# Kernel optimization log

Hardware: AMD Instinct MI355X
Metric: run time of the kernel (lower is better)

The kernel has to match this reference:

```python
import jax, jax.numpy as jnp
import numpy as np

IMG = 40  # imgSize hard-coded in FFTNet


def _fft_layer(z, w):
    # z: complex64 [B, inC, H, W]; w: float32 [inC, outC, H, W, 2]
    # torch.fft(..., 2, normalized=True) == 2D FFT with 'ortho' norm over last two dims
    F = jnp.fft.fft2(z, norm='ortho')
    wc = jax.lax.complex(w[..., 0], w[..., 1])
    # dft_conv: per-frequency complex multiply then sum over input channels
    # (Karatsuba trick in the original == plain complex multiply)
    mixed = jnp.einsum('bihw,iohw->bohw', F, wc)
    return jnp.fft.ifft2(mixed, norm='ortho')


def _crelu(z):
    # F.relu applied to the stacked [..., 2] real/imag tensor => relu each part
    return jax.lax.complex(jax.nn.relu(z.real), jax.nn.relu(z.imag))


def _fftnet(x, ws):
    # x: [B, 1, H, W] real; stacked with zeros -> complex input
    z = x.astype(jnp.complex64)
    for w in ws[:-1]:
        z = _crelu(_fft_layer(z, w))
    z = _fft_layer(z, ws[-1])
    return z.real  # x[..., 0]


def setup_inputs() -> dict:
    key = jax.random.key(0)
    ks = jax.random.split(key, 7)
    B = 256
    x = jax.random.normal(ks[0], (B, 1, IMG, IMG), dtype=jnp.float32)

    def make_w(k, i, o):
        # xavier_normal_ on torch shape (1, i, o, H, W, 2):
        # fan_in = i * (o*H*W*2), fan_out = 1 * (o*H*W*2)
        recept = o * IMG * IMG * 2
        std = float(np.sqrt(2.0 / (i * recept + recept)))
        return jax.random.normal(k, (i, o, IMG, IMG, 2), dtype=jnp.float32) * std

    chans = [(1, 40), (40, 40), (40, 40), (40, 40), (40, 40), (40, 1)]
    inp = {'x': x}
    for n, (k, (i, o)) in enumerate(zip(ks[1:], chans), start=1):
        inp[f'w{n}'] = make_w(k, i, o)
    return inp


def reference(x, w1, w2, w3, w4, w5, w6):
    return _fftnet(x, (w1, w2, w3, w4, w5, w6))
```

## Files before the change

kernel.cpp:

```cpp
#include <hip/hip_runtime.h>
#include <math.h>

#define NPIX 1600
#define NIMG 40
#define SW   40
#define PSZ  (48 * SW)

#define RST 322
#define OST 482

typedef __bf16 bf16x8 __attribute__((ext_vector_type(8)));
typedef float  f32x4  __attribute__((ext_vector_type(4)));
#define MFMA __builtin_amdgcn_mfma_f32_16x16x32_bf16

__device__ __forceinline__ unsigned short bits16(__bf16 x) {
    return __builtin_bit_cast(unsigned short, x);
}

__device__ __forceinline__ void cfma(float2& acc, float ax, float ay, float bx, float by) {
    acc.x = fmaf(ax, bx, fmaf(-ay, by, acc.x));
    acc.y = fmaf(ax, by, fmaf( ay, bx, acc.y));
}

__global__ void init_dtab(unsigned short* __restrict__ Dtab) {
    int idx = blockIdx.x * 256 + threadIdx.x;
    if (idx >= 2304) return;
    int rec = idx >> 6, lane = idx & 63;
    int p = rec % 6, t = (rec / 6) % 3, kc = rec / 18;
    unsigned short out[8];
    for (int j = 0; j < 8; ++j) {
        int k = kc * 32 + (lane >> 4) * 8 + j;
        int n = t * 16 + (lane & 15);
        float val = 0.0f;
        if (k < 40 && n < 40) {
            float ang = 6.28318530717958647692f * (float)((k * n) % 40) / 40.0f;
            float dr, di, s, c;
            sincosf(ang, &s, &c);
            dr = c; di = s;
            float base = (p < 2) ? dr : (p < 4) ? di : -di;
            __bf16 hi = (__bf16)base;
            if ((p & 1) == 0) val = (float)hi;
            else              val = (float)(__bf16)(base - (float)hi);
        }
        out[j] = __builtin_bit_cast(unsigned short, (__bf16)val);
    }
    unsigned short* dst = Dtab + (size_t)rec * 512 + lane * 8;
    for (int j = 0; j < 8; ++j) dst[j] = out[j];
}

template<bool REAL_IN, bool RELU, bool REAL_OUT>
__global__ __launch_bounds__(256) void fft2_kernel(const void* __restrict__ inv,
                                                   void* __restrict__ outv,
                                                   int dir)
{
    const int img = blockIdx.x;
    const int tid = threadIdx.x;
    __shared__ float2 A[NPIX];
    __shared__ float2 T[NPIX];
    __shared__ float2 D[NPIX];
    __shared__ float2 tw[NIMG];

    if (tid < NIMG) {
        float ang = (float)dir * 6.28318530717958647692f * (float)tid / 40.0f;
        float s, c;
        sincosf(ang, &s, &c);
        tw[tid] = make_float2(c, s);
    }
    if (REAL_IN) {
        const float* in = (const float*)inv + (size_t)img * NPIX;
        for (int idx = tid; idx < NPIX; idx += 256)
            A[idx] = make_float2(in[idx], 0.0f);
    } else {
        const float2* in = (const float2*)inv + (size_t)img * NPIX;
        for (int idx = tid; idx < NPIX; idx += 256)
            A[idx] = in[idx];
    }
    __syncthreads();
    for (int idx = tid; idx < NPIX; idx += 256) {
        int a = idx / NIMG, b = idx - a * NIMG;
        D[idx] = tw[(a * b) % NIMG];
    }
    __syncthreads();

    for (int idx = tid; idx < NPIX; idx += 256) {
        int h = idx / NIMG, v = idx - h * NIMG;
        float2 s = make_float2(0.0f, 0.0f);
        const float2* Arow = &A[h * NIMG];
        #pragma unroll
        for (int w = 0; w < NIMG; ++w) {
            float2 a = Arow[w];
            float2 d = D[w * NIMG + v];
            s.x += a.x * d.x - a.y * d.y;
            s.y += a.x * d.y + a.y * d.x;
        }
        T[idx] = s;
    }
    __syncthreads();

    for (int idx = tid; idx < NPIX; idx += 256) {
        int u = idx / NIMG, v = idx - u * NIMG;
        float2 s = make_float2(0.0f, 0.0f);
        const float2* Du = &D[u * NIMG];
        #pragma unroll
        for (int h = 0; h < NIMG; ++h) {
            float2 t = T[h * NIMG + v];
            float2 d = Du[h];
            s.x += t.x * d.x - t.y * d.y;
            s.y += t.x * d.y + t.y * d.x;
        }
        s.x *= 0.025f;
        s.y *= 0.025f;
        if (RELU) { s.x = fmaxf(s.x, 0.0f); s.y = fmaxf(s.y, 0.0f); }
        if (REAL_OUT) {
            ((float*)outv)[(size_t)img * NPIX + idx] = s.x;
        } else {
            ((float2*)outv)[(size_t)img * NPIX + idx] = s;
        }
    }
}

__device__ __forceinline__ void mac_row(f32x4& aR, f32x4& aI,
    bf16x8 xrh, bf16x8 xrl, bf16x8 xih, bf16x8 xil,
    bf16x8 drh, bf16x8 drl, bf16x8 dih, bf16x8 dil, bf16x8 dnh, bf16x8 dnl)
{
    aR = MFMA(xrh, drh, aR, 0, 0, 0);
    aR = MFMA(xrl, drh, aR, 0, 0, 0);
    aR = MFMA(xrh, drl, aR, 0, 0, 0);
    aR = MFMA(xih, dnh, aR, 0, 0, 0);
    aR = MFMA(xil, dnh, aR, 0, 0, 0);
    aR = MFMA(xih, dnl, aR, 0, 0, 0);
    aI = MFMA(xrh, dih, aI, 0, 0, 0);
    aI = MFMA(xrl, dih, aI, 0, 0, 0);
    aI = MFMA(xrh, dil, aI, 0, 0, 0);
    aI = MFMA(xih, drh, aI, 0, 0, 0);
    aI = MFMA(xil, drh, aI, 0, 0, 0);
    aI = MFMA(xih, drl, aI, 0, 0, 0);
}

__device__ __forceinline__ void mac_col(f32x4& aR, f32x4& aI,
    bf16x8 drh, bf16x8 drl, bf16x8 dih, bf16x8 dil, bf16x8 dnh, bf16x8 dnl,
    bf16x8 trh, bf16x8 trl, bf16x8 tih, bf16x8 til)
{
    aR = MFMA(drh, trh, aR, 0, 0, 0);
    aR = MFMA(drl, trh, aR, 0, 0, 0);
    aR = MFMA(drh, trl, aR, 0, 0, 0);
    aR = MFMA(dnh, tih, aR, 0, 0, 0);
    aR = MFMA(dnl, tih, aR, 0, 0, 0);
    aR = MFMA(dnh, til, aR, 0, 0, 0);
    aI = MFMA(drh, tih, aI, 0, 0, 0);
    aI = MFMA(drl, tih, aI, 0, 0, 0);
    aI = MFMA(drh, til, aI, 0, 0, 0);
    aI = MFMA(dih, trh, aI, 0, 0, 0);
    aI = MFMA(dil, trh, aI, 0, 0, 0);
    aI = MFMA(dih, trl, aI, 0, 0, 0);
}

__device__ __forceinline__ void mac_mix(f32x4& aR, f32x4& aI,
    bf16x8 frh, bf16x8 frl, bf16x8 fih, bf16x8 fil, bf16x8 fnih, bf16x8 fnil,
    bf16x8 wrh, bf16x8 wrl, bf16x8 wih, bf16x8 wil)
{
    aR = MFMA(frh,  wrh, aR, 0, 0, 0);
    aR = MFMA(frl,  wrh, aR, 0, 0, 0);
    aR = MFMA(frh,  wrl, aR, 0, 0, 0);
    aR = MFMA(fnih, wih, aR, 0, 0, 0);
    aR = MFMA(fnil, wih, aR, 0, 0, 0);
    aR = MFMA(fnih, wil, aR, 0, 0, 0);
    aI = MFMA(frh,  wih, aI, 0, 0, 0);
    aI = MFMA(frl,  wih, aI, 0, 0, 0);
    aI = MFMA(frh,  wil, aI, 0, 0, 0);
    aI = MFMA(fih,  wrh, aI, 0, 0, 0);
    aI = MFMA(fil,  wrh, aI, 0, 0, 0);
    aI = MFMA(fih,  wrl, aI, 0, 0, 0);
}

__global__ __launch_bounds__(512, 2) void mix_mfma_kernel(const float2* __restrict__ F,
                                                          const float2* __restrict__ W,
                                                          float2* __restrict__ M)
{
    __shared__ alignas(16) char smem[102912];
    float2* raw  = (float2*)smem;
    float2* outt = (float2*)(smem + 41216);
    float2* lw   = (float2*)smem;

    const int tid  = threadIdx.x;
    const int w    = tid >> 6;
    const int lane = tid & 63;
    const int q    = lane >> 4;
    const int m    = lane & 15;
    const int fw   = blockIdx.x >> 3;
    const int bg   = blockIdx.x & 7;
    const int f0   = fw * 8;
    const int fsub = w;

    f32x4 pf[5];
    #pragma unroll
    for (int k = 0; k < 5; ++k) {
        int c = tid + (k << 9);
        int r = c >> 2, sub = c & 3;
        int b = r / 40, i = r - b * 40;
        const f32x4* g = (const f32x4*)(F + ((size_t)((bg * 32 + b) * 40 + i) * NPIX + f0));
        pf[k] = __builtin_nontemporal_load(g + sub);
    }

    #pragma unroll
    for (int k = 0; k < 13; ++k) {
        int c = tid + (k << 9);
        if (c < 6400) {
            int r = c >> 2, sub = c & 3;
            const f32x4* g = (const f32x4*)(W + ((size_t)r * NPIX + f0));
            *(f32x4*)&lw[r * 8 + sub * 2] = g[sub];
        }
    }
    __syncthreads();

    bf16x8 wt[2][3][4];
    #pragma unroll
    for (int kc = 0; kc < 2; ++kc) {
        #pragma unroll
        for (int nt = 0; nt < 3; ++nt) {
            bf16x8 wrh = (bf16x8){}, wrl = (bf16x8){};
            bf16x8 wih = (bf16x8){}, wil = (bf16x8){};
            const int o = nt * 16 + m;
            const bool have = ((kc == 0) || (q == 0)) && (o < 40);
            if (have) {
                #pragma unroll
                for (int j = 0; j < 8; ++j) {
                    int i = kc * 32 + q * 8 + j;
                    float2 v = lw[(i * 40 + o) * 8 + fsub];
                    __bf16 h1 = (__bf16)v.x;
                    wrh[j] = h1; wrl[j] = (__bf16)(v.x - (float)h1);
                    __bf16 h2 = (__bf16)v.y;
                    wih[j] = h2; wil[j] = (__bf16)(v.y - (float)h2);
                }
            }
            wt[kc][nt][0] = wrh; wt[kc][nt][1] = wrl;
            wt[kc][nt][2] = wih; wt[kc][nt][3] = wil;
        }
    }
    __syncthreads();

    #pragma unroll
    for (int bt = 0; bt < 2; ++bt) {
        const int btile = bg * 2 + bt;

        #pragma unroll
        for (int k = 0; k < 5; ++k) {
            int c = tid + (k << 9);
            int r = c >> 2, sub = c & 3;
            int b = r / 40, i = r - b * 40;
            *(f32x4*)&raw[b * RST + i * 8 + sub * 2] = pf[k];
        }
        __syncthreads();

        if (bt == 0) {
            #pragma unroll
            for (int k = 0; k < 5; ++k) {
                int c = tid + (k << 9);
                int r = c >> 2, sub = c & 3;
                int b = r / 40, i = r - b * 40;
                const f32x4* g = (const f32x4*)(F + ((size_t)(((bg * 2 + 1) * 16 + b) * 40 + i) * NPIX + f0));
                pf[k] = __builtin_nontemporal_load(g + sub);
            }
        }

        f32x4 accR[3], accI[3];
        #pragma unroll
        for (int nt = 0; nt < 3; ++nt) {
            accR[nt] = (f32x4){0.f, 0.f, 0.f, 0.f};
            accI[nt] = (f32x4){0.f, 0.f, 0.f, 0.f};
        }

        #pragma unroll
        for (int kc = 0; kc < 2; ++kc) {
            const bool have = (kc == 0) || (q == 0);
            float re[8], im[8];
            #pragma unroll
            for (int j = 0; j < 8; ++j) {
                int i = kc * 32 + q * 8 + j;
                if (have) {
                    float2 v = raw[m * RST + i * 8 + fsub];
                    re[j] = v.x; im[j] = v.y;
                } else { re[j] = 0.f; im[j] = 0.f; }
            }
            bf16x8 frh, frl, fih, fil, fnih, fnil;
            #pragma unroll
            for (int j = 0; j < 8; ++j) {
                __bf16 h1 = (__bf16)re[j];
                frh[j] = h1;
                float lo = re[j] - (float)h1;
                frl[j] = (__bf16)lo;
                __bf16 h2 = (__bf16)im[j];
                fih[j] = h2;
                float lo2 = im[j] - (float)h2;
                fil[j] = (__bf16)lo2;
                fnih[j] = (__bf16)(-(float)h2);
                fnil[j] = (__bf16)(-lo2);
            }
            #pragma unroll
            for (int nt = 0; nt < 3; ++nt)
                mac_mix(accR[nt], accI[nt], frh, frl, fih, fil, fnih, fnil,
                        wt[kc][nt][0], wt[kc][nt][1], wt[kc][nt][2], wt[kc][nt][3]);
        }

        #pragma unroll
        for (int nt = 0; nt < 3; ++nt)
            #pragma unroll
            for (int g2 = 0; g2 < 4; ++g2)
                outt[(q * 4 + g2) * OST + (nt * 16 + m) * 10 + fsub] =
                    make_float2(accR[nt][g2], accI[nt][g2]);
        __syncthreads();

        #pragma unroll
        for (int k = 0; k < 5; ++k) {
            int c = tid + (k << 9);
            int r = c >> 2, sub = c & 3;
            int b = r / 40, o = r - b * 40;
            f32x4 v = *(const f32x4*)&outt[b * OST + o * 10 + sub * 2];
            f32x4* g = (f32x4*)(M + ((size_t)((btile * 16 + b) * 40 + o) * NPIX + f0));
            __builtin_nontemporal_store(v, g + sub);
        }
    }
}

__global__ __launch_bounds__(576, 5) void fused_mfma_kernel(const float2* __restrict__ in,
                                                            float2* __restrict__ outg,
                                                            const unsigned short* __restrict__ Dtab)
{
    __shared__ unsigned short Pl[4 * PSZ];
    __shared__ unsigned short Dlds[36 * 512];

    const int tid  = threadIdx.x;
    const int wv   = tid >> 6;
    const int lane = tid & 63;
    const int q    = lane >> 4;
    const int m    = lane & 15;
    const int mt   = wv / 3;
    const int nt   = wv - mt * 3;

    #pragma unroll
    for (int c = 0; c < 4; ++c) {
        int idx = c * 576 + tid;
        int rec = idx >> 6, l2 = idx & 63;
        *(f32x4*)&Dlds[rec * 512 + l2 * 8] =
            *(const f32x4*)(Dtab + (size_t)rec * 512 + l2 * 8);
    }

    #pragma unroll 1
    for (int ii = 0; ii < 5; ++ii) {
        const size_t img  = (size_t)blockIdx.x + (size_t)ii * 2048;
        const size_t base = img * NPIX;

        {
            const float4* src = (const float4*)(in + base);
            #pragma unroll
            for (int c = 0; c < 2; ++c) {
                int p = c * 576 + tid;
                if (p < 800) {
                    float4 v = src[p];
                    int h = p / 20, w2 = (p - h * 20) * 2;
                    int o = h * SW + w2;
                    __bf16 rh0 = (__bf16)v.x, ih0 = (__bf16)v.y;
                    __bf16 rh1 = (__bf16)v.z, ih1 = (__bf16)v.w;
                    ushort2 s0, s1, s2, s3;
                    s0.x = bits16(rh0); s0.y = bits16(rh1);
                    s1.x = bits16((__bf16)(v.x - (float)rh0));
                    s1.y = bits16((__bf16)(v.z - (float)rh1));
                    s2.x = bits16(ih0); s2.y = bits16(ih1);
                    s3.x = bits16((__bf16)(v.y - (float)ih0));
                    s3.y = bits16((__bf16)(v.w - (float)ih1));
                    *(ushort2*)&Pl[0 * PSZ + o] = s0;
                    *(ushort2*)&Pl[1 * PSZ + o] = s1;
                    *(ushort2*)&Pl[2 * PSZ + o] = s2;
                    *(ushort2*)&Pl[3 * PSZ + o] = s3;
                }
            }
            if (tid < 320) {
                int pl = tid / 80, rem = tid - pl * 80;
                int r = 40 + rem / 10, c4 = (rem - (rem / 10) * 10) * 4;
                *(ushort4*)&Pl[pl * PSZ + r * SW + c4] = make_ushort4(0, 0, 0, 0);
            }
        }
        __syncthreads();

        #pragma unroll
        for (int rep = 0; rep < 2; ++rep) {
            const int IP = rep ? 4 : 2;
            const int IN = rep ? 2 : 4;

            f32x4 aR = (f32x4){0.f, 0.f, 0.f, 0.f};
            f32x4 aI = (f32x4){0.f, 0.f, 0.f, 0.f};

            #pragma unroll
            for (int kc = 0; kc < 2; ++kc) {
                const bool have = (kc == 0) || (q == 0);
                bf16x8 xrh, xrl, xih, xil;
                if (have) {
                    int o = (mt * 16 + m) * SW + kc * 32 + q * 8;
                    xrh = *(const bf16x8*)&Pl[0 * PSZ + o];
                    xrl = *(const bf16x8*)&Pl[1 * PSZ + o];
                    xih = *(const bf16x8*)&Pl[2 * PSZ + o];
                    xil = *(const bf16x8*)&Pl[3 * PSZ + o];
                } else {
                    xrh = (bf16x8){}; xrl = (bf16x8){};
                    xih = (bf16x8){}; xil = (bf16x8){};
                }
                const int rb = (kc * 3 + nt) * 6;
                bf16x8 drh = *(const bf16x8*)&Dlds[(rb + 0) * 512 + lane * 8];
                bf16x8 drl = *(const bf16x8*)&Dlds[(rb + 1) * 512 + lane * 8];
                bf16x8 dih = *(const bf16x8*)&Dlds[(rb + IP) * 512 + lane * 8];
                bf16x8 dil = *(const bf16x8*)&Dlds[(rb + IP + 1) * 512 + lane * 8];
                bf16x8 dnh = *(const bf16x8*)&Dlds[(rb + IN) * 512 + lane * 8];
                bf16x8 dnl = *(const bf16x8*)&Dlds[(rb + IN + 1) * 512 + lane * 8];
                __builtin_amdgcn_s_setprio(1);
                mac_row(aR, aI, xrh, xrl, xih, xil,
                        drh, drl, dih, dil, dnh, dnl);
                __builtin_amdgcn_s_setprio(0);
            }
            __syncthreads();

            {
                int hb = mt * 16 + q * 4;
                if (hb < 40) {
                    int v = nt * 16 + m;
                    ushort4 srh, srl, sih, sil;
                    unsigned short* prh = (unsigned short*)&srh;
                    unsigned short* prl = (unsigned short*)&srl;
                    unsigned short* pih = (unsigned short*)&sih;
                    unsigned short* pil = (unsigned short*)&sil;
                    #pragma unroll
                    for (int g = 0; g < 4; ++g) {
                        __bf16 h1 = (__bf16)aR[g];
                        prh[g] = bits16(h1);
                        prl[g] = bits16((__bf16)(aR[g] - (float)h1));
                        __bf16 h2 = (__bf16)aI[g];
                        pih[g] = bits16(h2);
                        pil[g] = bits16((__bf16)(aI[g] - (float)h2));
                    }
                    int o = v * SW + hb;
                    *(ushort4*)&Pl[0 * PSZ + o] = srh;
                    *(ushort4*)&Pl[1 * PSZ + o] = srl;
                    *(ushort4*)&Pl[2 * PSZ + o] = sih;
                    *(ushort4*)&Pl[3 * PSZ + o] = sil;
                }
            }
            __syncthreads();

            aR = (f32x4){0.f, 0.f, 0.f, 0.f};
            aI = (f32x4){0.f, 0.f, 0.f, 0.f};

            #pragma unroll
            for (int kc = 0; kc < 2; ++kc) {
                const bool have = (kc == 0) || (q == 0);
                bf16x8 trh, trl, tih, til;
                if (have) {
                    int o = (nt * 16 + m) * SW + kc * 32 + q * 8;
                    trh = *(const bf16x8*)&Pl[0 * PSZ + o];
                    trl = *(const bf16x8*)&Pl[1 * PSZ + o];
                    tih = *(const bf16x8*)&Pl[2 * PSZ + o];
                    til = *(const bf16x8*)&Pl[3 * PSZ + o];
                } else {
                    trh = (bf16x8){}; trl = (bf16x8){};
                    tih = (bf16x8){}; til = (bf16x8){};
                }
                const int rb = (kc * 3 + mt) * 6;
                bf16x8 drh = *(const bf16x8*)&Dlds[(rb + 0) * 512 + lane * 8];
                bf16x8 drl = *(const bf16x8*)&Dlds[(rb + 1) * 512 + lane * 8];
                bf16x8 dih = *(const bf16x8*)&Dlds[(rb + IP) * 512 + lane * 8];
                bf16x8 dil = *(const bf16x8*)&Dlds[(rb + IP + 1) * 512 + lane * 8];
                bf16x8 dnh = *(const bf16x8*)&Dlds[(rb + IN) * 512 + lane * 8];
                bf16x8 dnl = *(const bf16x8*)&Dlds[(rb + IN + 1) * 512 + lane * 8];
                __builtin_amdgcn_s_setprio(1);
                mac_col(aR, aI, drh, drl, dih, dil, dnh, dnl,
                        trh, trl, tih, til);
                __builtin_amdgcn_s_setprio(0);
            }

            if (rep == 0) {
                __syncthreads();
                int v = nt * 16 + m;
                int u0 = mt * 16 + q * 4;
                if (v < 40 && u0 < 40) {
                    ushort4 srh, srl, sih, sil;
                    unsigned short* prh = (unsigned short*)&srh;
                    unsigned short* prl = (unsigned short*)&srl;
                    unsigned short* pih = (unsigned short*)&sih;
                    unsigned short* pil = (unsigned short*)&sil;
                    #pragma unroll
                    for (int g = 0; g < 4; ++g) {
                        float xr = fmaxf(aR[g] * 0.025f, 0.f);
                        float xi = fmaxf(aI[g] * 0.025f, 0.f);
                        __bf16 h1 = (__bf16)xr;
                        prh[g] = bits16(h1);
                        prl[g] = bits16((__bf16)(xr - (float)h1));
                        __bf16 h2 = (__bf16)xi;
                        pih[g] = bits16(h2);
                        pil[g] = bits16((__bf16)(xi - (float)h2));
                    }
                    int o = v * SW + u0;
                    *(ushort4*)&Pl[0 * PSZ + o] = srh;
                    *(ushort4*)&Pl[1 * PSZ + o] = srl;
                    *(ushort4*)&Pl[2 * PSZ + o] = sih;
                    *(ushort4*)&Pl[3 * PSZ + o] = sil;
                }
                __syncthreads();
            } else {
                float2* dst = outg + base;
                int v = nt * 16 + m;
                int u0 = mt * 16 + q * 4;
                if (v < 40 && u0 < 40) {
                    float4 s0, s1;
                    s0.x = aR[0] * 0.025f; s0.y = aI[0] * 0.025f;
                    s0.z = aR[1] * 0.025f; s0.w = aI[1] * 0.025f;
                    s1.x = aR[2] * 0.025f; s1.y = aI[2] * 0.025f;
                    s1.z = aR[3] * 0.025f; s1.w = aI[3] * 0.025f;
                    *(float4*)&dst[v * NIMG + u0]     = s0;
                    *(float4*)&dst[v * NIMG + u0 + 2] = s1;
                }
            }
        }
        __syncthreads();
    }
}

template<int INC, int OUTC, int BT, int OT>
__global__ __launch_bounds__(256) void mix_kernel(const float2* __restrict__ F,
                                                  const float2* __restrict__ W,
                                                  float2* __restrict__ M)
{
    const int tid = threadIdx.x;
    const int lane = tid & 63;
    const int wv = tid >> 6;
    const int f = (blockIdx.x % 25) * 64 + lane;
    const int bg = (blockIdx.x / 25) * 4 + wv;
    const int b0 = bg * BT;

    #pragma unroll
    for (int o0 = 0; o0 < OUTC; o0 += OT) {
        float2 acc[BT][OT];
        #pragma unroll
        for (int t = 0; t < BT; ++t)
            #pragma unroll
            for (int o = 0; o < OT; ++o)
                acc[t][o] = make_float2(0.0f, 0.0f);

        for (int i = 0; i < INC; ++i) {
            float2 fv[BT];
            #pragma unroll
            for (int t = 0; t < BT; ++t)
                fv[t] = F[((size_t)(b0 + t) * INC + i) * NPIX + f];
            float2 wr[OT];
            #pragma unroll
            for (int o = 0; o < OT; ++o)
                wr[o] = W[((size_t)i * OUTC + (o0 + o)) * NPIX + f];
            #pragma unroll
            for (int t = 0; t < BT; ++t)
                #pragma unroll
                for (int o = 0; o < OT; ++o)
                    cfma(acc[t][o], fv[t].x, fv[t].y, wr[o].x, wr[o].y);
        }
        #pragma unroll
        for (int t = 0; t < BT; ++t)
            #pragma unroll
            for (int o = 0; o < OT; ++o)
                M[((size_t)(b0 + t) * OUTC + (o0 + o)) * NPIX + f] = acc[t][o];
    }
}

extern "C" void kernel_launch(void* const* d_in, const int* in_sizes, int n_in,
                              void* d_out, int out_size, void* d_ws, size_t ws_size,
                              hipStream_t stream)
{
    const float* x = (const float*)d_in[0];
    const float2* w[6];
    for (int i = 0; i < 6; ++i) w[i] = (const float2*)d_in[1 + i];
    float* out = (float*)d_out;

    const size_t bufBytes = (size_t)256 * 40 * NPIX * sizeof(float2);
    float2* A = (float2*)d_ws;
    float2* B = (float2*)((char*)d_ws + bufBytes);
    unsigned short* Dtab = (unsigned short*)((char*)d_ws + 2 * bufBytes);

    const int FUSEGRID = 2048;
    const int MIXBLK = 25 * (256 / 4) / 4;

    init_dtab<<<9, 256, 0, stream>>>(Dtab);

    fft2_kernel<true, false, false><<<256, 256, 0, stream>>>(x, A, -1);

    mix_kernel<1, 40, 4, 10><<<MIXBLK, 256, 0, stream>>>(A, w[0], B);
    fused_mfma_kernel<<<FUSEGRID, 576, 0, stream>>>(B, A, Dtab);

    for (int l = 1; l <= 4; ++l) {
        mix_mfma_kernel<<<1600, 512, 0, stream>>>(A, w[l], B);
        fused_mfma_kernel<<<FUSEGRID, 576, 0, stream>>>(B, A, Dtab);
    }

    mix_kernel<40, 1, 4, 1><<<MIXBLK, 256, 0, stream>>>(A, w[5], B);
    fft2_kernel<false, false, true><<<256, 256, 0, stream>>>(B, out, +1);
}
```

Before: 1.415 ms.

## Keep DFT twiddle fragments in registers and split complex MACs into four real accumulators

The fused FFT kernel no longer stages the DFT twiddle table in shared memory. Each wave loads its eight bf16 twiddle fragments (hi/lo of real and imaginary parts) into registers once. The forward and inverse transforms now reuse those fragments through four separate real-product accumulators, and signs are combined at store time, so the negated-imaginary table and the per-iteration LDS loads are no longer needed. The wave-to-tile mapping is changed so the same twiddle fragment serves both row and column passes. This lowers LDS traffic and footprint at the cost of more VGPRs, and the launch bound drops from 5 to 4 blocks per CU.

Measured after the change: 1.384 ms. -2.2%, faster.

```diff
diff --git a/kernel.cpp b/kernel.cpp
--- a/kernel.cpp
+++ b/kernel.cpp
@@ -20,6 +20,14 @@
 __device__ __forceinline__ void cfma(float2& acc, float ax, float ay, float bx, float by) {
     acc.x = fmaf(ax, bx, fmaf(-ay, by, acc.x));
     acc.y = fmaf(ax, by, fmaf( ay, bx, acc.y));
+}
+
+__device__ __forceinline__ void mac3(f32x4& acc, bf16x8 ah, bf16x8 al,
+                                     bf16x8 bh, bf16x8 bl)
+{
+    acc = MFMA(ah, bh, acc, 0, 0, 0);
+    acc = MFMA(al, bh, acc, 0, 0, 0);
+    acc = MFMA(ah, bl, acc, 0, 0, 0);
 }
 
 __global__ void init_dtab(unsigned short* __restrict__ Dtab) {
@@ -119,42 +127,6 @@
     }
 }
 
-__device__ __forceinline__ void mac_row(f32x4& aR, f32x4& aI,
-    bf16x8 xrh, bf16x8 xrl, bf16x8 xih, bf16x8 xil,
-    bf16x8 drh, bf16x8 drl, bf16x8 dih, bf16x8 dil, bf16x8 dnh, bf16x8 dnl)
-{
-    aR = MFMA(xrh, drh, aR, 0, 0, 0);
-    aR = MFMA(xrl, drh, aR, 0, 0, 0);
-    aR = MFMA(xrh, drl, aR, 0, 0, 0);
-    aR = MFMA(xih, dnh, aR, 0, 0, 0);
-    aR = MFMA(xil, dnh, aR, 0, 0, 0);
-    aR = MFMA(xih, dnl, aR, 0, 0, 0);
-    aI = MFMA(xrh, dih, aI, 0, 0, 0);
-    aI = MFMA(xrl, dih, aI, 0, 0, 0);
-    aI = MFMA(xrh, dil, aI, 0, 0, 0);
-    aI = MFMA(xih, drh, aI, 0, 0, 0);
-    aI = MFMA(xil, drh, aI, 0, 0, 0);
-    aI = MFMA(xih, drl, aI, 0, 0, 0);
-}
-
-__device__ __forceinline__ void mac_col(f32x4& aR, f32x4& aI,
-    bf16x8 drh, bf16x8 drl, bf16x8 dih, bf16x8 dil, bf16x8 dnh, bf16x8 dnl,
-    bf16x8 trh, bf16x8 trl, bf16x8 tih, bf16x8 til)
-{
-    aR = MFMA(drh, trh, aR, 0, 0, 0);
-    aR = MFMA(drl, trh, aR, 0, 0, 0);
-    aR = MFMA(drh, trl, aR, 0, 0, 0);
-    aR = MFMA(dnh, tih, aR, 0, 0, 0);
-    aR = MFMA(dnl, tih, aR, 0, 0, 0);
-    aR = MFMA(dnh, til, aR, 0, 0, 0);
-    aI = MFMA(drh, tih, aI, 0, 0, 0);
-    aI = MFMA(drl, tih, aI, 0, 0, 0);
-    aI = MFMA(drh, til, aI, 0, 0, 0);
-    aI = MFMA(dih, trh, aI, 0, 0, 0);
-    aI = MFMA(dil, trh, aI, 0, 0, 0);
-    aI = MFMA(dih, trl, aI, 0, 0, 0);
-}
-
 __device__ __forceinline__ void mac_mix(f32x4& aR, f32x4& aI,
     bf16x8 frh, bf16x8 frl, bf16x8 fih, bf16x8 fil, bf16x8 fnih, bf16x8 fnil,
     bf16x8 wrh, bf16x8 wrl, bf16x8 wih, bf16x8 wil)
@@ -322,28 +294,26 @@
     }
 }
 
-__global__ __launch_bounds__(576, 5) void fused_mfma_kernel(const float2* __restrict__ in,
+__global__ __launch_bounds__(576, 4) void fused_mfma_kernel(const float2* __restrict__ in,
                                                             float2* __restrict__ outg,
                                                             const unsigned short* __restrict__ Dtab)
 {
     __shared__ unsigned short Pl[4 * PSZ];
-    __shared__ unsigned short Dlds[36 * 512];
 
     const int tid  = threadIdx.x;
     const int wv   = tid >> 6;
     const int lane = tid & 63;
     const int q    = lane >> 4;
     const int m    = lane & 15;
-    const int mt   = wv / 3;
-    const int nt   = wv - mt * 3;
-
+    const int a    = wv / 3;
+    const int b    = wv - a * 3;
+
+    bf16x8 dd[2][4];
     #pragma unroll
-    for (int c = 0; c < 4; ++c) {
-        int idx = c * 576 + tid;
-        int rec = idx >> 6, l2 = idx & 63;
-        *(f32x4*)&Dlds[rec * 512 + l2 * 8] =
-            *(const f32x4*)(Dtab + (size_t)rec * 512 + l2 * 8);
-    }
+    for (int kc = 0; kc < 2; ++kc)
+        #pragma unroll
+        for (int p = 0; p < 4; ++p)
+            dd[kc][p] = ((const bf16x8*)Dtab)[((size_t)(kc * 3 + b) * 6 + p) * 64 + lane];
 
     #pragma unroll 1
     for (int ii = 0; ii < 5; ++ii) {
@@ -384,18 +354,16 @@
 
         #pragma unroll
         for (int rep = 0; rep < 2; ++rep) {
-            const int IP = rep ? 4 : 2;
-            const int IN = rep ? 2 : 4;
-
-            f32x4 aR = (f32x4){0.f, 0.f, 0.f, 0.f};
-            f32x4 aI = (f32x4){0.f, 0.f, 0.f, 0.f};
+
+            f32x4 P1 = (f32x4){0.f,0.f,0.f,0.f}, P2 = (f32x4){0.f,0.f,0.f,0.f};
+            f32x4 P3 = (f32x4){0.f,0.f,0.f,0.f}, P4 = (f32x4){0.f,0.f,0.f,0.f};
 
             #pragma unroll
             for (int kc = 0; kc < 2; ++kc) {
                 const bool have = (kc == 0) || (q == 0);
                 bf16x8 xrh, xrl, xih, xil;
                 if (have) {
-                    int o = (mt * 16 + m) * SW + kc * 32 + q * 8;
+                    int o = (a * 16 + m) * SW + kc * 32 + q * 8;
                     xrh = *(const bf16x8*)&Pl[0 * PSZ + o];
                     xrl = *(const bf16x8*)&Pl[1 * PSZ + o];
                     xih = *(const bf16x8*)&Pl[2 * PSZ + o];
@@ -404,24 +372,19 @@
                     xrh = (bf16x8){}; xrl = (bf16x8){};
                     xih = (bf16x8){}; xil = (bf16x8){};
                 }
-                const int rb = (kc * 3 + nt) * 6;
-                bf16x8 drh = *(const bf16x8*)&Dlds[(rb + 0) * 512 + lane * 8];
-                bf16x8 drl = *(const bf16x8*)&Dlds[(rb + 1) * 512 + lane * 8];
-                bf16x8 dih = *(const bf16x8*)&Dlds[(rb + IP) * 512 + lane * 8];
-                bf16x8 dil = *(const bf16x8*)&Dlds[(rb + IP + 1) * 512 + lane * 8];
-                bf16x8 dnh = *(const bf16x8*)&Dlds[(rb + IN) * 512 + lane * 8];
-                bf16x8 dnl = *(const bf16x8*)&Dlds[(rb + IN + 1) * 512 + lane * 8];
                 __builtin_amdgcn_s_setprio(1);
-                mac_row(aR, aI, xrh, xrl, xih, xil,
-                        drh, drl, dih, dil, dnh, dnl);
+                mac3(P1, xrh, xrl, dd[kc][0], dd[kc][1]);
+                mac3(P2, xih, xil, dd[kc][2], dd[kc][3]);
+                mac3(P3, xrh, xrl, dd[kc][2], dd[kc][3]);
+                mac3(P4, xih, xil, dd[kc][0], dd[kc][1]);
                 __builtin_amdgcn_s_setprio(0);
             }
             __syncthreads();
 
             {
-                int hb = mt * 16 + q * 4;
+                int hb = a * 16 + q * 4;
                 if (hb < 40) {
-                    int v = nt * 16 + m;
+                    int v = b * 16 + m;
                     ushort4 srh, srl, sih, sil;
                     unsigned short* prh = (unsigned short*)&srh;
                     unsigned short* prl = (unsigned short*)&srl;
@@ -429,12 +392,15 @@
                     unsigned short* pil = (unsigned short*)&sil;
                     #pragma unroll
                     for (int g = 0; g < 4; ++g) {
-                        __bf16 h1 = (__bf16)aR[g];
+                        float tR, tI;
+                        if (rep == 0) { tR = P1[g] - P2[g]; tI = P3[g] + P4[g]; }
+                        else          { tR = P1[g] + P2[g]; tI = P4[g] - P3[g]; }
+                        __bf16 h1 = (__bf16)tR;
                         prh[g] = bits16(h1);
-                        prl[g] = bits16((__bf16)(aR[g] - (float)h1));
-                        __bf16 h2 = (__bf16)aI[g];
+                        prl[g] = bits16((__bf16)(tR - (float)h1));
+                        __bf16 h2 = (__bf16)tI;
                         pih[g] = bits16(h2);
-                        pil[g] = bits16((__bf16)(aI[g] - (float)h2));
+                        pil[g] = bits16((__bf16)(tI - (float)h2));
                     }
                     int o = v * SW + hb;
                     *(ushort4*)&Pl[0 * PSZ + o] = srh;
@@ -445,15 +411,15 @@
             }
             __syncthreads();
 
-            aR = (f32x4){0.f, 0.f, 0.f, 0.f};
-            aI = (f32x4){0.f, 0.f, 0.f, 0.f};
+            P1 = (f32x4){0.f,0.f,0.f,0.f}; P2 = (f32x4){0.f,0.f,0.f,0.f};
+            P3 = (f32x4){0.f,0.f,0.f,0.f}; P4 = (f32x4){0.f,0.f,0.f,0.f};
 
             #pragma unroll
             for (int kc = 0; kc < 2; ++kc) {
                 const bool have = (kc == 0) || (q == 0);
                 bf16x8 trh, trl, tih, til;
                 if (have) {
-                    int o = (nt * 16 + m) * SW + kc * 32 + q * 8;
+                    int o = (a * 16 + m) * SW + kc * 32 + q * 8;
                     trh = *(const bf16x8*)&Pl[0 * PSZ + o];
                     trl = *(const bf16x8*)&Pl[1 * PSZ + o];
                     tih = *(const bf16x8*)&Pl[2 * PSZ + o];
@@ -462,23 +428,18 @@
                     trh = (bf16x8){}; trl = (bf16x8){};
                     tih = (bf16x8){}; til = (bf16x8){};
                 }
-                const int rb = (kc * 3 + mt) * 6;
-                bf16x8 drh = *(const bf16x8*)&Dlds[(rb + 0) * 512 + lane * 8];
-                bf16x8 drl = *(const bf16x8*)&Dlds[(rb + 1) * 512 + lane * 8];
-                bf16x8 dih = *(const bf16x8*)&Dlds[(rb + IP) * 512 + lane * 8];
-                bf16x8 dil = *(const bf16x8*)&Dlds[(rb + IP + 1) * 512 + lane * 8];
-                bf16x8 dnh = *(const bf16x8*)&Dlds[(rb + IN) * 512 + lane * 8];
-                bf16x8 dnl = *(const bf16x8*)&Dlds[(rb + IN + 1) * 512 + lane * 8];
                 __builtin_amdgcn_s_setprio(1);
-                mac_col(aR, aI, drh, drl, dih, dil, dnh, dnl,
-                        trh, trl, tih, til);
+                mac3(P1, dd[kc][0], dd[kc][1], trh, trl);
+                mac3(P2, dd[kc][2], dd[kc][3], tih, til);
+                mac3(P3, dd[kc][0], dd[kc][1], tih, til);
+                mac3(P4, dd[kc][2], dd[kc][3], trh, trl);
                 __builtin_amdgcn_s_setprio(0);
             }
 
             if (rep == 0) {
                 __syncthreads();
-                int v = nt * 16 + m;
-                int u0 = mt * 16 + q * 4;
+                int v = a * 16 + m;
+                int u0 = b * 16 + q * 4;
                 if (v < 40 && u0 < 40) {
                     ushort4 srh, srl, sih, sil;
                     unsigned short* prh = (unsigned short*)&srh;
@@ -487,8 +448,10 @@
                     unsigned short* pil = (unsigned short*)&sil;
                     #pragma unroll
                     for (int g = 0; g < 4; ++g) {
-                        float xr = fmaxf(aR[g] * 0.025f, 0.f);
-                        float xi = fmaxf(aI[g] * 0.025f, 0.f);
+                        float cR = P1[g] - P2[g];
+                        float cI = P3[g] + P4[g];
+                        float xr = fmaxf(cR * 0.025f, 0.f);
+                        float xi = fmaxf(cI * 0.025f, 0.f);
                         __bf16 h1 = (__bf16)xr;
                         prh[g] = bits16(h1);
                         prl[g] = bits16((__bf16)(xr - (float)h1));
@@ -505,14 +468,18 @@
                 __syncthreads();
             } else {
                 float2* dst = outg + base;
-                int v = nt * 16 + m;
-                int u0 = mt * 16 + q * 4;
+                int v = a * 16 + m;
+                int u0 = b * 16 + q * 4;
                 if (v < 40 && u0 < 40) {
                     float4 s0, s1;
-                    s0.x = aR[0] * 0.025f; s0.y = aI[0] * 0.025f;
-                    s0.z = aR[1] * 0.025f; s0.w = aI[1] * 0.025f;
-                    s1.x = aR[2] * 0.025f; s1.y = aI[2] * 0.025f;
-                    s1.z = aR[3] * 0.025f; s1.w = aI[3] * 0.025f;
+                    float r0 = P1[0] + P2[0], i0 = P3[0] - P4[0];
+                    float r1 = P1[1] + P2[1], i1 = P3[1] - P4[1];
+                    float r2 = P1[2] + P2[2], i2 = P3[2] - P4[2];
+                    float r3 = P1[3] + P2[3], i3 = P3[3] - P4[3];
+                    s0.x = r0 * 0.025f; s0.y = i0 * 0.025f;
+                    s0.z = r1 * 0.025f; s0.w = i1 * 0.025f;
+                    s1.x = r2 * 0.025f; s1.y = i2 * 0.025f;
+                    s1.z = r3 * 0.025f; s1.w = i3 * 0.025f;
                     *(float4*)&dst[v * NIMG + u0]     = s0;
                     *(float4*)&dst[v * NIMG + u0 + 2] = s1;
                 }
```
